# Kernel tuning notes

Measured on AMD Instinct MI355X. Metric: run time of the kernel, lower is better.

## Reference

```python
import jax, jax.numpy as jnp
import numpy as np

C_FEAT = 512
HID = 256
OUT = 3
IN_DIM = C_FEAT + 2 + 2  # feat + rel_coord + rel_cell = 516


def _nearest_idx(g, size):
    # grid_sample nearest, align_corners=False: unnormalize then round (half-to-even)
    x = ((g + 1.0) * size - 1.0) / 2.0
    return jnp.clip(jnp.round(x).astype(jnp.int32), 0, size - 1)


def setup_inputs() -> dict:
    key = jax.random.key(0)
    ks = jax.random.split(key, 12)
    B, Q, H, W = 2, 65536, 48, 48
    feat = jax.random.normal(ks[0], (B, C_FEAT, H, W), dtype=jnp.float32)
    coord = jax.random.uniform(ks[1], (B, Q, 2), dtype=jnp.float32, minval=-1.0, maxval=1.0)
    cell = jnp.full((B, Q, 2), 2.0 / 256.0, dtype=jnp.float32)  # query at 256x256 output res
    def lin_init(k, fan_in, fan_out):
        s = 1.0 / np.sqrt(fan_in)
        return jax.random.uniform(k, (fan_in, fan_out), jnp.float32, -s, s)
    W0 = lin_init(ks[2], IN_DIM, HID); b0 = jnp.zeros((HID,), jnp.float32)
    W1 = lin_init(ks[3], HID, HID);    b1 = jnp.zeros((HID,), jnp.float32)
    W2 = lin_init(ks[4], HID, HID);    b2 = jnp.zeros((HID,), jnp.float32)
    W3 = lin_init(ks[5], HID, HID);    b3 = jnp.zeros((HID,), jnp.float32)
    W4 = lin_init(ks[6], HID, OUT);    b4 = jnp.zeros((OUT,), jnp.float32)
    return {"feat": feat, "coord": coord, "cell": cell,
            "W0": W0, "b0": b0, "W1": W1, "b1": b1, "W2": W2, "b2": b2,
            "W3": W3, "b3": b3, "W4": W4, "b4": b4}


def _liif(feat, coord, cell, W0, b0, W1, b1, W2, b2, W3, b3, W4, b4):
    B, C, H, W = feat.shape
    Q = coord.shape[1]
    rx = 1.0 / H  # 2 / H / 2
    ry = 1.0 / W
    eps = 1e-6
    # local ensemble shifts (vx, vy) in order [(-1,-1),(-1,1),(1,-1),(1,1)]
    shifts = jnp.array([[-1., -1.], [-1., 1.], [1., -1.], [1., 1.]], dtype=feat.dtype)
    off = shifts * jnp.array([rx, ry], dtype=feat.dtype) + eps  # [4,2]
    coord_s = jnp.clip(coord[None] + off[:, None, None, :], -1 + 1e-6, 1 - 1e-6)  # [4,B,Q,2]
    # coord[...,0] indexes H (rows), coord[...,1] indexes W (cols) [code flips before grid_sample]
    idx_r = _nearest_idx(coord_s[..., 0], H)  # [4,B,Q]
    idx_c = _nearest_idx(coord_s[..., 1], W)
    lin = idx_r * W + idx_c                   # [4,B,Q]
    flat = feat.reshape(B, C, H * W).transpose(0, 2, 1)  # [B,HW,C]
    q_feat = jnp.take_along_axis(flat[None], lin[..., None], axis=2)  # [4,B,Q,C]
    # feat_coord grid_sample == center coord of the gathered cell
    qc_r = (idx_r.astype(feat.dtype) + 0.5) * (2.0 / H) - 1.0
    qc_c = (idx_c.astype(feat.dtype) + 0.5) * (2.0 / W) - 1.0
    rel = jnp.stack([(coord[None, ..., 0] - qc_r) * H,
                     (coord[None, ..., 1] - qc_c) * W], axis=-1)  # [4,B,Q,2]
    rel_cell = cell * jnp.array([H, W], dtype=feat.dtype)          # [B,Q,2]
    rel_cell4 = jnp.broadcast_to(rel_cell[None], (4, B, Q, 2))
    inp = jnp.concatenate([q_feat, rel, rel_cell4], axis=-1)       # [4,B,Q,516]
    # shared per-point MLP
    h = jax.nn.relu(inp @ W0 + b0)
    h = jax.nn.relu(h @ W1 + b1)
    h = jax.nn.relu(h @ W2 + b2)
    h = jax.nn.relu(h @ W3 + b3)
    pred = h @ W4 + b4                                             # [4,B,Q,3]
    area = jnp.abs(rel[..., 0] * rel[..., 1]) + 1e-9               # [4,B,Q]
    tot = area.sum(axis=0)
    # swap areas 0<->3 and 1<->2 (diagonal weighting) == reverse
    w = area[::-1] / tot[None]
    return (pred * w[..., None]).sum(axis=0)                       # [B,Q,3]


def reference(feat, coord, cell, W0, b0, W1, b1, W2, b2, W3, b3, W4, b4):
    return _liif(feat, coord, cell, W0, b0, W1, b1, W2, b2, W3, b3, W4, b4)
```

## Files before the change

kernel.cpp:

```cpp
#include <hip/hip_runtime.h>
#include <hip/hip_bf16.h>
#include <math.h>

#define HH    48
#define CFEAT 512
#define HID   256
#define NPOS  (HH*HH)
#define TQ    48
#define NEV   192
#define NB    1366

typedef __attribute__((ext_vector_type(8))) short bf16x8;
typedef __attribute__((ext_vector_type(4))) float f32x4;

static __device__ __forceinline__ unsigned short f2bf(float x) {
  unsigned int u = __float_as_uint(x);
  u += 0x7fffu + ((u >> 16) & 1u);
  return (unsigned short)(u >> 16);
}

static __device__ __forceinline__ unsigned int pk2bf(float a, float b) {
  __hip_bfloat162 h2 = __float22bfloat162_rn(make_float2(a, b));
  unsigned int u; __builtin_memcpy(&u, &h2, 4); return u;
}

static __device__ __forceinline__ void rel_calc(float c0, float c1, int s,
                                                float& r0, float& r1,
                                                int& ir, int& ic) {
  float vx = (s & 2) ? 1.0f : -1.0f;
  float vy = (s & 1) ? 1.0f : -1.0f;
  const float RXY = (float)(1.0/48.0);
  const float CLO = (float)(-1.0 + 1e-6);
  const float CHI = (float)( 1.0 - 1e-6);
  float gx = __fadd_rn(c0, __fadd_rn(__fmul_rn(vx, RXY), 1e-6f));
  float gy = __fadd_rn(c1, __fadd_rn(__fmul_rn(vy, RXY), 1e-6f));
  gx = fminf(fmaxf(gx, CLO), CHI);
  gy = fminf(fmaxf(gy, CLO), CHI);
  float xr = __fmul_rn(__fsub_rn(__fmul_rn(__fadd_rn(gx, 1.0f), 48.0f), 1.0f), 0.5f);
  float xc = __fmul_rn(__fsub_rn(__fmul_rn(__fadd_rn(gy, 1.0f), 48.0f), 1.0f), 0.5f);
  ir = (int)rintf(xr); ir = ir < 0 ? 0 : (ir > HH-1 ? HH-1 : ir);
  ic = (int)rintf(xc); ic = ic < 0 ? 0 : (ic > HH-1 ? HH-1 : ic);
  const float T2 = (float)(2.0/48.0);
  float qcr = __fsub_rn(__fmul_rn(__fadd_rn((float)ir, 0.5f), T2), 1.0f);
  float qcc = __fsub_rn(__fmul_rn(__fadd_rn((float)ic, 0.5f), T2), 1.0f);
  r0 = __fmul_rn(__fsub_rn(c0, qcr), 48.0f);
  r1 = __fmul_rn(__fsub_rn(c1, qcc), 48.0f);
}

__global__ __launch_bounds__(256) void liif_precompute(
    const float* __restrict__ feat, const float* __restrict__ W0,
    const float* __restrict__ b0, float* __restrict__ P)
{
  int blk = blockIdx.x;
  int b   = blk / (NPOS/4);
  int p0  = (blk - b*(NPOS/4)) * 4;
  int n   = threadIdx.x;
  const float* f = feat + (size_t)b * CFEAT * NPOS + p0;
  float bias = b0[n];
  float a0 = bias, a1 = bias, a2 = bias, a3 = bias;
  #pragma unroll 4
  for (int c = 0; c < CFEAT; ++c) {
    float w = W0[c*HID + n];
    const float* fr = f + (size_t)c * NPOS;
    a0 += fr[0]*w; a1 += fr[1]*w; a2 += fr[2]*w; a3 += fr[3]*w;
  }
  float* Pp = P + ((size_t)b*NPOS + p0)*HID + n;
  Pp[0*HID] = a0; Pp[1*HID] = a1; Pp[2*HID] = a2; Pp[3*HID] = a3;
}

__global__ __launch_bounds__(256) void liif_convert(
    const float* __restrict__ W1, const float* __restrict__ W2,
    const float* __restrict__ W3, const float* __restrict__ W4,
    unsigned char* __restrict__ img, unsigned char* __restrict__ w4i)
{
  int blk = blockIdx.x, t = threadIdx.x;
  if (blk < 24) {
    int l = blk >> 3, kc = blk & 7;
    const float* W = (l == 0) ? W1 : (l == 1) ? W2 : W3;
    unsigned short* dst = (unsigned short*)(img + (size_t)blk * 16384);
    #pragma unroll 1
    for (int s = 0; s < 4; ++s) {
      int p    = t + s*256;
      int wc   = p >> 8;
      int nt   = (p >> 6) & 3;
      int lane = p & 63;
      int lr   = lane & 15, lk = lane >> 4;
      int n    = wc*64 + nt*16 + lr;
      int k0   = kc*32 + lk*8;
      #pragma unroll
      for (int j = 0; j < 8; ++j)
        dst[p*8 + j] = f2bf(W[(k0 + j)*256 + n]);
    }
  } else {
    unsigned short* dst = (unsigned short*)w4i;
    #pragma unroll
    for (int u = 0; u < 2; ++u) {
      int p    = t + u*256;
      int kc   = p >> 6;
      int lane = p & 63;
      int n    = lane & 15;
      int k0   = kc*32 + (lane >> 4)*8;
      #pragma unroll
      for (int j = 0; j < 8; ++j)
        dst[p*8 + j] = (n < 3) ? f2bf(W4[(k0 + j)*3 + n]) : (unsigned short)0;
    }
  }
}


#define WBASE  98304

#define MF(A, B, C) __builtin_amdgcn_mfma_f32_16x16x32_bf16((A), (B), (C), 0, 0, 0)

#define AS1(p) ((const __attribute__((address_space(1))) void*)(unsigned long long)(const void*)(p))
#define AS3(p) ((__attribute__((address_space(3))) void*)(unsigned int)(unsigned long long)(void*)(p))

#define STAGEG(GOFF, BUF) do {                                                \
    __builtin_amdgcn_global_load_lds(                                         \
        AS1(img + (GOFF) + sgoff),                                            \
        AS3(lds + WBASE + (BUF)*32768 + swoff), 16, 0, 0);                    \
    __builtin_amdgcn_global_load_lds(                                         \
        AS1(img + (GOFF) + 12288 + sgoff),                                    \
        AS3(lds + WBASE + (BUF)*32768 + 12288 + swoff), 16, 0, 0);            \
    if (w < 8)                                                                \
      __builtin_amdgcn_global_load_lds(                                       \
          AS1(img + (GOFF) + 24576 + sgoff),                                  \
          AS3(lds + WBASE + (BUF)*32768 + 24576 + swoff), 16, 0, 0);          \
  } while (0)

#define KSTEPC(KC) do {                                                       \
    const unsigned char* wb_ = lds + WBASE + (((KC) >> 1) & 1)*32768          \
                             + (((KC) & 1)*16384) + lwoff;                    \
    bf16x8 w0_ = *(const bf16x8*)(wb_ + 0);                                   \
    bf16x8 w1_ = *(const bf16x8*)(wb_ + 1024);                                \
    bf16x8 w2_ = *(const bf16x8*)(wb_ + 2048);                                \
    bf16x8 w3_ = *(const bf16x8*)(wb_ + 3072);                                \
    const int ko_ = (((KC) << 6) ^ xb6);                                      \
    bf16x8 a0_ = *(const bf16x8*)(lds + rb0 + ko_);                           \
    bf16x8 a1_ = *(const bf16x8*)(lds + rb1 + ko_);                           \
    bf16x8 a2_ = *(const bf16x8*)(lds + rb2 + ko_);                           \
    bf16x8 a3_ = *(const bf16x8*)(lds + rb3 + ko_);                           \
    acc[0]  = MF(w0_, a0_, acc[0]);  acc[1]  = MF(w1_, a0_, acc[1]);          \
    acc[2]  = MF(w2_, a0_, acc[2]);  acc[3]  = MF(w3_, a0_, acc[3]);          \
    acc[4]  = MF(w0_, a1_, acc[4]);  acc[5]  = MF(w1_, a1_, acc[5]);          \
    acc[6]  = MF(w2_, a1_, acc[6]);  acc[7]  = MF(w3_, a1_, acc[7]);          \
    acc[8]  = MF(w0_, a2_, acc[8]);  acc[9]  = MF(w1_, a2_, acc[9]);          \
    acc[10] = MF(w2_, a2_, acc[10]); acc[11] = MF(w3_, a2_, acc[11]);         \
    acc[12] = MF(w0_, a3_, acc[12]); acc[13] = MF(w1_, a3_, acc[13]);         \
    acc[14] = MF(w2_, a3_, acc[14]); acc[15] = MF(w3_, a3_, acc[15]);         \
  } while (0)

#define LGROUP(G, HASN, NGOFF) do {                                           \
    if (HASN) STAGEG((NGOFF), (((G)+1)&1));                                   \
    KSTEPC(2*(G)); KSTEPC(2*(G)+1);                                           \
    __syncthreads();                                                          \
  } while (0)

#define LAYERC3(LOFF, NLOFF) do {                                             \
    _Pragma("unroll")                                                         \
    for (int i_ = 0; i_ < 16; ++i_) acc[i_] = (f32x4){0.f, 0.f, 0.f, 0.f};    \
    LGROUP(0, 1, (LOFF) + 32768);                                             \
    LGROUP(1, 1, (LOFF) + 65536);                                             \
    LGROUP(2, 1, (LOFF) + 98304);                                             \
    LGROUP(3, 1, (NLOFF));                                                    \
  } while (0)

#define LAYER_WB3(BIAS) do {                                                  \
    _Pragma("unroll")                                                         \
    for (int nt_ = 0; nt_ < 4; ++nt_) {                                       \
      f32x4 bv_ = *(const f32x4*)&(BIAS)[nW + nt_*16 + lk*4];                 \
      const int cb_ = (cwb + nt_*32) ^ xwb;                                   \
      _Pragma("unroll")                                                       \
      for (int mt_ = 0; mt_ < 4; ++mt_) {                                     \
        f32x4 a_ = acc[mt_*4 + nt_];                                          \
        unsigned int lo_ = pk2bf(fmaxf(a_[0] + bv_[0], 0.f),                  \
                                 fmaxf(a_[1] + bv_[1], 0.f));                 \
        unsigned int hi_ = pk2bf(fmaxf(a_[2] + bv_[2], 0.f),                  \
                                 fmaxf(a_[3] + bv_[3], 0.f));                 \
        *(uint2*)(lds + ((m0 + mt_*16 + lr) << 9) + cb_) = make_uint2(lo_, hi_); \
      }                                                                       \
    }                                                                         \
  } while (0)

__global__ __launch_bounds__(768, 3)
__attribute__((amdgpu_waves_per_eu(3, 3)))
void liif_main(
    const float* __restrict__ coord, const float* __restrict__ cell,
    const float* __restrict__ P,  const float* __restrict__ W0,
    const unsigned char* __restrict__ img,
    const unsigned char* __restrict__ w4i,
    const float* __restrict__ b1, const float* __restrict__ b2,
    const float* __restrict__ b3, const float* __restrict__ b4,
    float* __restrict__ out)
{
  __shared__ __align__(16) unsigned char lds[163840];
  int*   lin_s = (int*)  (lds + WBASE);
  f32x4* rel4  = (f32x4*)(lds + WBASE + 1024);
  float* predp = (float*)lds;

  const int t   = threadIdx.x;
  const int blk = blockIdx.x;
  const int b   = (blk >= NB) ? 1 : 0;
  const int q0  = (blk - b*NB) * TQ;

  const int lane = t & 63;
  const int w    = t >> 6;
  const int m0   = (w >> 2) * 64;
  const int wc   = w & 3;
  const int nW   = wc * 64;
  const int lr   = lane & 15;
  const int lk   = lane >> 4;

  const size_t sgoff = (size_t)t * 16;
  const int    swoff = w * 1024;

  const int lwoff = wc*4096 + lane*16;
  const int xl  = (lr & 3) << 4;
  const int xb6 = ((lr >> 2) & 1) << 6;
  const int rb0 = ((m0 +  0 + lr) << 9) + ((lk << 4) ^ xl);
  const int rb1 = ((m0 + 16 + lr) << 9) + ((lk << 4) ^ xl);
  const int rb2 = ((m0 + 32 + lr) << 9) + ((lk << 4) ^ xl);
  const int rb3 = ((m0 + 48 + lr) << 9) + ((lk << 4) ^ xl);
  const int cwb = wc*128 + lk*8;
  const int xwb = (lr & 7) << 4;

  if (t < NEV) {
    const int e = t;
    int q = q0 + (e >> 2);
    if (q > 65535) q = 65535;
    const int s = e & 3;
    const size_t cbase = (((size_t)b << 16) + q) * 2;
    float c0 = coord[cbase + 0];
    float c1 = coord[cbase + 1];
    float r0, r1; int ir, ic;
    rel_calc(c0, c1, s, r0, r1, ir, ic);
    lin_s[e] = ir*HH + ic;
    rel4[e] = (f32x4){r0, r1,
                      __fmul_rn(cell[cbase + 0], 48.0f),
                      __fmul_rn(cell[cbase + 1], 48.0f)};
  }
  __syncthreads();

  {
    const int cg = lane;
    const float* w0t = W0 + (size_t)512*HID + cg*4;
    f32x4 wr0 = *(const f32x4*)(w0t);
    f32x4 wr1 = *(const f32x4*)(w0t + 256);
    f32x4 wr2 = *(const f32x4*)(w0t + 512);
    f32x4 wr3 = *(const f32x4*)(w0t + 768);
    const float* Pb = P + (size_t)b * NPOS * HID + cg*4;
    const int wb = cg * 8;
    #pragma unroll 2
    for (int i = 0; i < 16; ++i) {
      const int e = w*16 + i;
      const int lin = lin_s[e];
      f32x4 rel = rel4[e];
      f32x4 pv = *(const f32x4*)(Pb + (size_t)lin*HID);
      float v0 = pv[0] + rel[0]*wr0[0] + rel[1]*wr1[0] + rel[2]*wr2[0] + rel[3]*wr3[0];
      float v1 = pv[1] + rel[0]*wr0[1] + rel[1]*wr1[1] + rel[2]*wr2[1] + rel[3]*wr3[1];
      float v2 = pv[2] + rel[0]*wr0[2] + rel[1]*wr1[2] + rel[2]*wr2[2] + rel[3]*wr3[2];
      float v3 = pv[3] + rel[0]*wr0[3] + rel[1]*wr1[3] + rel[2]*wr2[3] + rel[3]*wr3[3];
      unsigned int lo = pk2bf(fmaxf(v0, 0.f), fmaxf(v1, 0.f));
      unsigned int hi = pk2bf(fmaxf(v2, 0.f), fmaxf(v3, 0.f));
      *(uint2*)(lds + (e << 9) + (wb ^ ((e & 7) << 4))) = make_uint2(lo, hi);
    }
  }
  __syncthreads();

  STAGEG(0, 0);
  __syncthreads();

  f32x4 acc[16];
  LAYERC3(0, 131072);
  LAYER_WB3(b1);
  __syncthreads();

  LAYERC3(131072, 262144);
  LAYER_WB3(b2);
  __syncthreads();

  {
    #pragma unroll
    for (int i_ = 0; i_ < 16; ++i_) acc[i_] = (f32x4){0.f, 0.f, 0.f, 0.f};
    LGROUP(0, 1, 262144 + 32768);
    LGROUP(1, 1, 262144 + 65536);
    LGROUP(2, 1, 262144 + 98304);
    if (w < 8)
      __builtin_amdgcn_global_load_lds(AS1(w4i + sgoff),
                                       AS3(lds + WBASE + swoff), 16, 0, 0);
    KSTEPC(6); KSTEPC(7);
    __syncthreads();
  }
  LAYER_WB3(b3);
  __syncthreads();

  {
    f32x4 acc4 = (f32x4){0.f, 0.f, 0.f, 0.f};
    const int fr_ = ((w << 4) + lr) << 9;
    #pragma unroll
    for (int kc = 0; kc < 8; ++kc) {
      bf16x8 wf = *(const bf16x8*)(lds + WBASE + kc*1024 + lane*16);
      bf16x8 af = *(const bf16x8*)(lds + fr_ + ((kc << 6) ^ xb6) + ((lk << 4) ^ xl));
      acc4 = MF(wf, af, acc4);
    }
    __syncthreads();
    if (lk == 0) {
      float* pp = predp + ((w << 4) + lr)*3;
      pp[0] = acc4[0] + b4[0];
      pp[1] = acc4[1] + b4[1];
      pp[2] = acc4[2] + b4[2];
    }
  }
  __syncthreads();

  if (t < TQ*3) {
    const int q = t / 3, o = t - (t/3)*3;
    const int qq = q0 + q;
    if (qq < 65536) {
      const int eb = q*4;
      const size_t cbase = (((size_t)b << 16) + qq) * 2;
      float c0 = coord[cbase + 0];
      float c1 = coord[cbase + 1];
      float ar[4];
      #pragma unroll
      for (int s = 0; s < 4; ++s) {
        float r0, r1; int ir, ic;
        rel_calc(c0, c1, s, r0, r1, ir, ic);
        ar[s] = __fadd_rn(fabsf(__fmul_rn(r0, r1)), 1e-9f);
      }
      float p0 = predp[(eb+0)*3 + o];
      float p1 = predp[(eb+1)*3 + o];
      float p2 = predp[(eb+2)*3 + o];
      float p3 = predp[(eb+3)*3 + o];
      float tot = ((ar[0] + ar[1]) + ar[2]) + ar[3];
      float rv = (p0*ar[3] + p1*ar[2] + p2*ar[1] + p3*ar[0]) / tot;
      out[(((size_t)b << 16) + qq)*3 + o] = rv;
    }
  }
}

extern "C" void kernel_launch(void* const* d_in, const int* in_sizes, int n_in,
                              void* d_out, int out_size, void* d_ws, size_t ws_size,
                              hipStream_t stream)
{
  const float* feat  = (const float*)d_in[0];
  const float* coord = (const float*)d_in[1];
  const float* cell  = (const float*)d_in[2];
  const float* W0    = (const float*)d_in[3];
  const float* b0    = (const float*)d_in[4];
  const float* W1    = (const float*)d_in[5];
  const float* b1    = (const float*)d_in[6];
  const float* W2    = (const float*)d_in[7];
  const float* b2    = (const float*)d_in[8];
  const float* W3    = (const float*)d_in[9];
  const float* b3    = (const float*)d_in[10];
  const float* W4    = (const float*)d_in[11];
  const float* b4    = (const float*)d_in[12];
  float* outp = (float*)d_out;

  float*         P    = (float*)d_ws;
  unsigned char* imgp = (unsigned char*)d_ws + 4718592;
  unsigned char* w4ip = (unsigned char*)d_ws + 4718592 + 393216;

  hipLaunchKernelGGL(liif_precompute, dim3(2*(NPOS/4)), dim3(256), 0, stream,
                     feat, W0, b0, P);
  hipLaunchKernelGGL(liif_convert, dim3(25), dim3(256), 0, stream,
                     W1, W2, W3, W4, imgp, w4ip);
  hipLaunchKernelGGL(liif_main, dim3(2*NB), dim3(768), 0, stream,
                     coord, cell, P, W0, imgp, w4ip, b1, b2, b3, b4, outp);
}
```

Before: 280.6 us.

## Retile main MLP kernel to 64 queries, 8 waves, 64x128 per-wave tiles

Changes the query tile from 48 to 64 points (256 evaluations), so blocks divide the query count evenly and bounds checks can be removed. Each of 8 waves now computes a 64x128 output tile with 32 accumulators, where it used to be 12 waves doing 64x64 tiles. Weight staging becomes per-k-step double buffering of 16KB chunks, issued before the first-layer gather so it overlaps that phase. The intent is more MFMA work per LDS weight load and fewer waves contending. The cost is higher register pressure, occupancy dropping to 2 waves/EU, and a sync after every k-step.

```diff
diff --git a/kernel.cpp b/kernel.cpp
--- a/kernel.cpp
+++ b/kernel.cpp
@@ -6,9 +6,8 @@
 #define CFEAT 512
 #define HID   256
 #define NPOS  (HH*HH)
-#define TQ    48
-#define NEV   192
-#define NB    1366
+#define TQ    64
+#define NEV   256
 
 typedef __attribute__((ext_vector_type(8))) short bf16x8;
 typedef __attribute__((ext_vector_type(4))) float f32x4;
@@ -108,33 +107,33 @@
 }
 
 
-#define WBASE  98304
+#define LDSW   131072
 
 #define MF(A, B, C) __builtin_amdgcn_mfma_f32_16x16x32_bf16((A), (B), (C), 0, 0, 0)
 
 #define AS1(p) ((const __attribute__((address_space(1))) void*)(unsigned long long)(const void*)(p))
 #define AS3(p) ((__attribute__((address_space(3))) void*)(unsigned int)(unsigned long long)(void*)(p))
 
-#define STAGEG(GOFF, BUF) do {                                                \
+#define STAGE2(LOFF, NKC, BUF) do {                                           \
     __builtin_amdgcn_global_load_lds(                                         \
-        AS1(img + (GOFF) + sgoff),                                            \
-        AS3(lds + WBASE + (BUF)*32768 + swoff), 16, 0, 0);                    \
+        AS1(img + (LOFF) + (NKC)*16384 + sgoff),                              \
+        AS3(lds + LDSW + (BUF)*16384 + swoff), 16, 0, 0);                     \
     __builtin_amdgcn_global_load_lds(                                         \
-        AS1(img + (GOFF) + 12288 + sgoff),                                    \
-        AS3(lds + WBASE + (BUF)*32768 + 12288 + swoff), 16, 0, 0);            \
-    if (w < 8)                                                                \
-      __builtin_amdgcn_global_load_lds(                                       \
-          AS1(img + (GOFF) + 24576 + sgoff),                                  \
-          AS3(lds + WBASE + (BUF)*32768 + 24576 + swoff), 16, 0, 0);          \
+        AS1(img + (LOFF) + (NKC)*16384 + sgoff + 8192),                       \
+        AS3(lds + LDSW + (BUF)*16384 + swoff + 8192), 16, 0, 0);              \
   } while (0)
 
-#define KSTEPC(KC) do {                                                       \
-    const unsigned char* wb_ = lds + WBASE + (((KC) >> 1) & 1)*32768          \
-                             + (((KC) & 1)*16384) + lwoff;                    \
+#define KSTEP32(KC, HASN, NLOFF, NKC) do {                                    \
+    if (HASN) STAGE2((NLOFF), (NKC), (((KC)+1)&1));                           \
+    const unsigned char* wb_ = lds + LDSW + (((KC)&1)*16384) + lwoff;         \
     bf16x8 w0_ = *(const bf16x8*)(wb_ + 0);                                   \
     bf16x8 w1_ = *(const bf16x8*)(wb_ + 1024);                                \
     bf16x8 w2_ = *(const bf16x8*)(wb_ + 2048);                                \
     bf16x8 w3_ = *(const bf16x8*)(wb_ + 3072);                                \
+    bf16x8 w4_ = *(const bf16x8*)(wb_ + 4096);                                \
+    bf16x8 w5_ = *(const bf16x8*)(wb_ + 5120);                                \
+    bf16x8 w6_ = *(const bf16x8*)(wb_ + 6144);                                \
+    bf16x8 w7_ = *(const bf16x8*)(wb_ + 7168);                                \
     const int ko_ = (((KC) << 6) ^ xb6);                                      \
     bf16x8 a0_ = *(const bf16x8*)(lds + rb0 + ko_);                           \
     bf16x8 a1_ = *(const bf16x8*)(lds + rb1 + ko_);                           \
@@ -142,37 +141,40 @@
     bf16x8 a3_ = *(const bf16x8*)(lds + rb3 + ko_);                           \
     acc[0]  = MF(w0_, a0_, acc[0]);  acc[1]  = MF(w1_, a0_, acc[1]);          \
     acc[2]  = MF(w2_, a0_, acc[2]);  acc[3]  = MF(w3_, a0_, acc[3]);          \
-    acc[4]  = MF(w0_, a1_, acc[4]);  acc[5]  = MF(w1_, a1_, acc[5]);          \
-    acc[6]  = MF(w2_, a1_, acc[6]);  acc[7]  = MF(w3_, a1_, acc[7]);          \
-    acc[8]  = MF(w0_, a2_, acc[8]);  acc[9]  = MF(w1_, a2_, acc[9]);          \
-    acc[10] = MF(w2_, a2_, acc[10]); acc[11] = MF(w3_, a2_, acc[11]);         \
-    acc[12] = MF(w0_, a3_, acc[12]); acc[13] = MF(w1_, a3_, acc[13]);         \
-    acc[14] = MF(w2_, a3_, acc[14]); acc[15] = MF(w3_, a3_, acc[15]);         \
-  } while (0)
-
-#define LGROUP(G, HASN, NGOFF) do {                                           \
-    if (HASN) STAGEG((NGOFF), (((G)+1)&1));                                   \
-    KSTEPC(2*(G)); KSTEPC(2*(G)+1);                                           \
+    acc[4]  = MF(w4_, a0_, acc[4]);  acc[5]  = MF(w5_, a0_, acc[5]);          \
+    acc[6]  = MF(w6_, a0_, acc[6]);  acc[7]  = MF(w7_, a0_, acc[7]);          \
+    acc[8]  = MF(w0_, a1_, acc[8]);  acc[9]  = MF(w1_, a1_, acc[9]);          \
+    acc[10] = MF(w2_, a1_, acc[10]); acc[11] = MF(w3_, a1_, acc[11]);         \
+    acc[12] = MF(w4_, a1_, acc[12]); acc[13] = MF(w5_, a1_, acc[13]);         \
+    acc[14] = MF(w6_, a1_, acc[14]); acc[15] = MF(w7_, a1_, acc[15]);         \
+    acc[16] = MF(w0_, a2_, acc[16]); acc[17] = MF(w1_, a2_, acc[17]);         \
+    acc[18] = MF(w2_, a2_, acc[18]); acc[19] = MF(w3_, a2_, acc[19]);         \
+    acc[20] = MF(w4_, a2_, acc[20]); acc[21] = MF(w5_, a2_, acc[21]);         \
+    acc[22] = MF(w6_, a2_, acc[22]); acc[23] = MF(w7_, a2_, acc[23]);         \
+    acc[24] = MF(w0_, a3_, acc[24]); acc[25] = MF(w1_, a3_, acc[25]);         \
+    acc[26] = MF(w2_, a3_, acc[26]); acc[27] = MF(w3_, a3_, acc[27]);         \
+    acc[28] = MF(w4_, a3_, acc[28]); acc[29] = MF(w5_, a3_, acc[29]);         \
+    acc[30] = MF(w6_, a3_, acc[30]); acc[31] = MF(w7_, a3_, acc[31]);         \
     __syncthreads();                                                          \
   } while (0)
 
-#define LAYERC3(LOFF, NLOFF) do {                                             \
+#define LAYER32(LOFF, NLOFF) do {                                             \
     _Pragma("unroll")                                                         \
-    for (int i_ = 0; i_ < 16; ++i_) acc[i_] = (f32x4){0.f, 0.f, 0.f, 0.f};    \
-    LGROUP(0, 1, (LOFF) + 32768);                                             \
-    LGROUP(1, 1, (LOFF) + 65536);                                             \
-    LGROUP(2, 1, (LOFF) + 98304);                                             \
-    LGROUP(3, 1, (NLOFF));                                                    \
+    for (int i_ = 0; i_ < 32; ++i_) acc[i_] = (f32x4){0.f, 0.f, 0.f, 0.f};    \
+    KSTEP32(0, 1, (LOFF), 1); KSTEP32(1, 1, (LOFF), 2);                       \
+    KSTEP32(2, 1, (LOFF), 3); KSTEP32(3, 1, (LOFF), 4);                       \
+    KSTEP32(4, 1, (LOFF), 5); KSTEP32(5, 1, (LOFF), 6);                       \
+    KSTEP32(6, 1, (LOFF), 7); KSTEP32(7, 1, (NLOFF), 0);                      \
   } while (0)
 
-#define LAYER_WB3(BIAS) do {                                                  \
+#define LAYER_WB(BIAS) do {                                                   \
     _Pragma("unroll")                                                         \
-    for (int nt_ = 0; nt_ < 4; ++nt_) {                                       \
+    for (int nt_ = 0; nt_ < 8; ++nt_) {                                       \
       f32x4 bv_ = *(const f32x4*)&(BIAS)[nW + nt_*16 + lk*4];                 \
       const int cb_ = (cwb + nt_*32) ^ xwb;                                   \
       _Pragma("unroll")                                                       \
       for (int mt_ = 0; mt_ < 4; ++mt_) {                                     \
-        f32x4 a_ = acc[mt_*4 + nt_];                                          \
+        f32x4 a_ = acc[mt_*8 + nt_];                                          \
         unsigned int lo_ = pk2bf(fmaxf(a_[0] + bv_[0], 0.f),                  \
                                  fmaxf(a_[1] + bv_[1], 0.f));                 \
         unsigned int hi_ = pk2bf(fmaxf(a_[2] + bv_[2], 0.f),                  \
@@ -182,8 +184,8 @@
     }                                                                         \
   } while (0)
 
-__global__ __launch_bounds__(768, 3)
-__attribute__((amdgpu_waves_per_eu(3, 3)))
+__global__ __launch_bounds__(512, 2)
+__attribute__((amdgpu_waves_per_eu(2, 2)))
 void liif_main(
     const float* __restrict__ coord, const float* __restrict__ cell,
     const float* __restrict__ P,  const float* __restrict__ W0,
@@ -194,40 +196,38 @@
     float* __restrict__ out)
 {
   __shared__ __align__(16) unsigned char lds[163840];
-  int*   lin_s = (int*)  (lds + WBASE);
-  f32x4* rel4  = (f32x4*)(lds + WBASE + 1024);
+  int*   lin_s = (int*)  (lds + 147456);
+  f32x4* rel4  = (f32x4*)(lds + 147456 + 1024);
   float* predp = (float*)lds;
 
   const int t   = threadIdx.x;
   const int blk = blockIdx.x;
-  const int b   = (blk >= NB) ? 1 : 0;
-  const int q0  = (blk - b*NB) * TQ;
+  const int b   = blk >> 10;
+  const int q0  = (blk & 1023) * TQ;
 
   const int lane = t & 63;
   const int w    = t >> 6;
-  const int m0   = (w >> 2) * 64;
-  const int wc   = w & 3;
-  const int nW   = wc * 64;
+  const int m0   = (w >> 1) * 64;
+  const int nW   = (w & 1) * 128;
   const int lr   = lane & 15;
   const int lk   = lane >> 4;
 
   const size_t sgoff = (size_t)t * 16;
   const int    swoff = w * 1024;
 
-  const int lwoff = wc*4096 + lane*16;
+  const int lwoff = (w & 1)*8192 + lane*16;
   const int xl  = (lr & 3) << 4;
   const int xb6 = ((lr >> 2) & 1) << 6;
   const int rb0 = ((m0 +  0 + lr) << 9) + ((lk << 4) ^ xl);
   const int rb1 = ((m0 + 16 + lr) << 9) + ((lk << 4) ^ xl);
   const int rb2 = ((m0 + 32 + lr) << 9) + ((lk << 4) ^ xl);
   const int rb3 = ((m0 + 48 + lr) << 9) + ((lk << 4) ^ xl);
-  const int cwb = wc*128 + lk*8;
+  const int cwb = (w & 1)*256 + lk*8;
   const int xwb = (lr & 7) << 4;
 
   if (t < NEV) {
     const int e = t;
-    int q = q0 + (e >> 2);
-    if (q > 65535) q = 65535;
+    const int q = q0 + (e >> 2);
     const int s = e & 3;
     const size_t cbase = (((size_t)b << 16) + q) * 2;
     float c0 = coord[cbase + 0];
@@ -241,6 +241,8 @@
   }
   __syncthreads();
 
+  STAGE2(0, 0, 0);
+
   {
     const int cg = lane;
     const float* w0t = W0 + (size_t)512*HID + cg*4;
@@ -251,8 +253,8 @@
     const float* Pb = P + (size_t)b * NPOS * HID + cg*4;
     const int wb = cg * 8;
     #pragma unroll 2
-    for (int i = 0; i < 16; ++i) {
-      const int e = w*16 + i;
+    for (int i = 0; i < 32; ++i) {
+      const int e = w*32 + i;
       const int lin = lin_s[e];
       f32x4 rel = rel4[e];
       f32x4 pv = *(const f32x4*)(Pb + (size_t)lin*HID);
@@ -267,75 +269,73 @@
   }
   __syncthreads();
 
-  STAGEG(0, 0);
-  __syncthreads();
-
-  f32x4 acc[16];
-  LAYERC3(0, 131072);
-  LAYER_WB3(b1);
-  __syncthreads();
-
-  LAYERC3(131072, 262144);
-  LAYER_WB3(b2);
+  f32x4 acc[32];
+  LAYER32(0, 131072);
+  LAYER_WB(b1);
+  __syncthreads();
+
+  LAYER32(131072, 262144);
+  LAYER_WB(b2);
   __syncthreads();
 
   {
     #pragma unroll
-    for (int i_ = 0; i_ < 16; ++i_) acc[i_] = (f32x4){0.f, 0.f, 0.f, 0.f};
-    LGROUP(0, 1, 262144 + 32768);
-    LGROUP(1, 1, 262144 + 65536);
-    LGROUP(2, 1, 262144 + 98304);
-    if (w < 8)
-      __builtin_amdgcn_global_load_lds(AS1(w4i + sgoff),
-                                       AS3(lds + WBASE + swoff), 16, 0, 0);
-    KSTEPC(6); KSTEPC(7);
-    __syncthreads();
-  }
-  LAYER_WB3(b3);
+    for (int i_ = 0; i_ < 32; ++i_) acc[i_] = (f32x4){0.f, 0.f, 0.f, 0.f};
+    KSTEP32(0, 1, 262144, 1); KSTEP32(1, 1, 262144, 2);
+    KSTEP32(2, 1, 262144, 3); KSTEP32(3, 1, 262144, 4);
+    KSTEP32(4, 1, 262144, 5); KSTEP32(5, 1, 262144, 6);
+    KSTEP32(6, 1, 262144, 7);
+    __builtin_amdgcn_global_load_lds(AS1(w4i + sgoff),
+                                     AS3(lds + LDSW + swoff), 16, 0, 0);
+    KSTEP32(7, 0, 0, 0);
+  }
+  LAYER_WB(b3);
   __syncthreads();
 
   {
-    f32x4 acc4 = (f32x4){0.f, 0.f, 0.f, 0.f};
-    const int fr_ = ((w << 4) + lr) << 9;
+    f32x4 acc4a = (f32x4){0.f, 0.f, 0.f, 0.f};
+    f32x4 acc4b = (f32x4){0.f, 0.f, 0.f, 0.f};
+    const int fr0 = ((w*32)      + lr) << 9;
+    const int fr1 = ((w*32 + 16) + lr) << 9;
     #pragma unroll
     for (int kc = 0; kc < 8; ++kc) {
-      bf16x8 wf = *(const bf16x8*)(lds + WBASE + kc*1024 + lane*16);
-      bf16x8 af = *(const bf16x8*)(lds + fr_ + ((kc << 6) ^ xb6) + ((lk << 4) ^ xl));
-      acc4 = MF(wf, af, acc4);
+      bf16x8 wf = *(const bf16x8*)(lds + LDSW + kc*1024 + lane*16);
+      const int ko = ((kc << 6) ^ xb6) + ((lk << 4) ^ xl);
+      bf16x8 afa = *(const bf16x8*)(lds + fr0 + ko);
+      bf16x8 afb = *(const bf16x8*)(lds + fr1 + ko);
+      acc4a = MF(wf, afa, acc4a);
+      acc4b = MF(wf, afb, acc4b);
     }
     __syncthreads();
     if (lk == 0) {
-      float* pp = predp + ((w << 4) + lr)*3;
-      pp[0] = acc4[0] + b4[0];
-      pp[1] = acc4[1] + b4[1];
-      pp[2] = acc4[2] + b4[2];
+      float* pa = predp + (w*32 + lr)*3;
+      float* pb = predp + (w*32 + 16 + lr)*3;
+      pa[0] = acc4a[0] + b4[0]; pa[1] = acc4a[1] + b4[1]; pa[2] = acc4a[2] + b4[2];
+      pb[0] = acc4b[0] + b4[0]; pb[1] = acc4b[1] + b4[1]; pb[2] = acc4b[2] + b4[2];
     }
   }
   __syncthreads();
 
   if (t < TQ*3) {
     const int q = t / 3, o = t - (t/3)*3;
-    const int qq = q0 + q;
-    if (qq < 65536) {
-      const int eb = q*4;
-      const size_t cbase = (((size_t)b << 16) + qq) * 2;
-      float c0 = coord[cbase + 0];
-      float c1 = coord[cbase + 1];
-      float ar[4];
-      #pragma unroll
-      for (int s = 0; s < 4; ++s) {
-        float r0, r1; int ir, ic;
-        rel_calc(c0, c1, s, r0, r1, ir, ic);
-        ar[s] = __fadd_rn(fabsf(__fmul_rn(r0, r1)), 1e-9f);
-      }
-      float p0 = predp[(eb+0)*3 + o];
-      float p1 = predp[(eb+1)*3 + o];
-      float p2 = predp[(eb+2)*3 + o];
-      float p3 = predp[(eb+3)*3 + o];
-      float tot = ((ar[0] + ar[1]) + ar[2]) + ar[3];
-      float rv = (p0*ar[3] + p1*ar[2] + p2*ar[1] + p3*ar[0]) / tot;
-      out[(((size_t)b << 16) + qq)*3 + o] = rv;
-    }
+    const int eb = q*4;
+    const size_t cbase = (((size_t)b << 16) + (q0 + q)) * 2;
+    float c0 = coord[cbase + 0];
+    float c1 = coord[cbase + 1];
+    float ar[4];
+    #pragma unroll
+    for (int s = 0; s < 4; ++s) {
+      float r0, r1; int ir, ic;
+      rel_calc(c0, c1, s, r0, r1, ir, ic);
+      ar[s] = __fadd_rn(fabsf(__fmul_rn(r0, r1)), 1e-9f);
+    }
+    float p0 = predp[(eb+0)*3 + o];
+    float p1 = predp[(eb+1)*3 + o];
+    float p2 = predp[(eb+2)*3 + o];
+    float p3 = predp[(eb+3)*3 + o];
+    float tot = ((ar[0] + ar[1]) + ar[2]) + ar[3];
+    float rv = (p0*ar[3] + p1*ar[2] + p2*ar[1] + p3*ar[0]) / tot;
+    out[(((size_t)b << 16) + (q0 + q))*3 + o] = rv;
   }
 }
 
@@ -366,6 +366,6 @@
                      feat, W0, b0, P);
   hipLaunchKernelGGL(liif_convert, dim3(25), dim3(256), 0, stream,
                      W1, W2, W3, W4, imgp, w4ip);
-  hipLaunchKernelGGL(liif_main, dim3(2*NB), dim3(768), 0, stream,
+  hipLaunchKernelGGL(liif_main, dim3(2048), dim3(512), 0, stream,
                      coord, cell, P, W0, imgp, w4ip, b1, b2, b3, b4, outp);
 }
```

Result: slower. 298.4 us (+6.3%).

## Software-pipeline MLP layers with per-k-chunk weight staging and register double-buffering

Applied to the files above, without the earlier changes.

Restructures the hidden-layer GEMM loop so weights are staged one 16KB k-chunk at a time into a two-slot LDS ring, while fragments for the next chunk are loaded into registers (even/odd sets) as the MFMAs for the current chunk issue. MFMA blocks are wrapped in s_setprio raises, and the first layer's weight staging is issued before the layer-0 gather so it overlaps that work. LDS use drops from 160KB to 128KB, but the change doubles the number of barriers per layer and adds register pressure from the extra fragment buffers.

```diff
diff --git a/kernel.cpp b/kernel.cpp
--- a/kernel.cpp
+++ b/kernel.cpp
@@ -108,64 +108,47 @@
 }
 
 
-#define WBASE  98304
+#define LDSW   98304
 
 #define MF(A, B, C) __builtin_amdgcn_mfma_f32_16x16x32_bf16((A), (B), (C), 0, 0, 0)
 
 #define AS1(p) ((const __attribute__((address_space(1))) void*)(unsigned long long)(const void*)(p))
 #define AS3(p) ((__attribute__((address_space(3))) void*)(unsigned int)(unsigned long long)(void*)(p))
 
-#define STAGEG(GOFF, BUF) do {                                                \
+#define STAGEC(LOFF, KC, BUF) do {                                            \
     __builtin_amdgcn_global_load_lds(                                         \
-        AS1(img + (GOFF) + sgoff),                                            \
-        AS3(lds + WBASE + (BUF)*32768 + swoff), 16, 0, 0);                    \
-    __builtin_amdgcn_global_load_lds(                                         \
-        AS1(img + (GOFF) + 12288 + sgoff),                                    \
-        AS3(lds + WBASE + (BUF)*32768 + 12288 + swoff), 16, 0, 0);            \
-    if (w < 8)                                                                \
+        AS1(img + (LOFF) + (KC)*16384 + sgoff),                               \
+        AS3(lds + LDSW + (BUF)*16384 + swoff), 16, 0, 0);                     \
+    if (w < 4)                                                                \
       __builtin_amdgcn_global_load_lds(                                       \
-          AS1(img + (GOFF) + 24576 + sgoff),                                  \
-          AS3(lds + WBASE + (BUF)*32768 + 24576 + swoff), 16, 0, 0);          \
-  } while (0)
-
-#define KSTEPC(KC) do {                                                       \
-    const unsigned char* wb_ = lds + WBASE + (((KC) >> 1) & 1)*32768          \
-                             + (((KC) & 1)*16384) + lwoff;                    \
-    bf16x8 w0_ = *(const bf16x8*)(wb_ + 0);                                   \
-    bf16x8 w1_ = *(const bf16x8*)(wb_ + 1024);                                \
-    bf16x8 w2_ = *(const bf16x8*)(wb_ + 2048);                                \
-    bf16x8 w3_ = *(const bf16x8*)(wb_ + 3072);                                \
-    const int ko_ = (((KC) << 6) ^ xb6);                                      \
-    bf16x8 a0_ = *(const bf16x8*)(lds + rb0 + ko_);                           \
-    bf16x8 a1_ = *(const bf16x8*)(lds + rb1 + ko_);                           \
-    bf16x8 a2_ = *(const bf16x8*)(lds + rb2 + ko_);                           \
-    bf16x8 a3_ = *(const bf16x8*)(lds + rb3 + ko_);                           \
-    acc[0]  = MF(w0_, a0_, acc[0]);  acc[1]  = MF(w1_, a0_, acc[1]);          \
-    acc[2]  = MF(w2_, a0_, acc[2]);  acc[3]  = MF(w3_, a0_, acc[3]);          \
-    acc[4]  = MF(w0_, a1_, acc[4]);  acc[5]  = MF(w1_, a1_, acc[5]);          \
-    acc[6]  = MF(w2_, a1_, acc[6]);  acc[7]  = MF(w3_, a1_, acc[7]);          \
-    acc[8]  = MF(w0_, a2_, acc[8]);  acc[9]  = MF(w1_, a2_, acc[9]);          \
-    acc[10] = MF(w2_, a2_, acc[10]); acc[11] = MF(w3_, a2_, acc[11]);         \
-    acc[12] = MF(w0_, a3_, acc[12]); acc[13] = MF(w1_, a3_, acc[13]);         \
-    acc[14] = MF(w2_, a3_, acc[14]); acc[15] = MF(w3_, a3_, acc[15]);         \
-  } while (0)
-
-#define LGROUP(G, HASN, NGOFF) do {                                           \
-    if (HASN) STAGEG((NGOFF), (((G)+1)&1));                                   \
-    KSTEPC(2*(G)); KSTEPC(2*(G)+1);                                           \
-    __syncthreads();                                                          \
-  } while (0)
-
-#define LAYERC3(LOFF, NLOFF) do {                                             \
+          AS1(img + (LOFF) + (KC)*16384 + 12288 + sgoff),                     \
+          AS3(lds + LDSW + (BUF)*16384 + 12288 + swoff), 16, 0, 0);           \
+  } while (0)
+
+#define RD(AARR, WARR, KC) do {                                               \
+    const unsigned char* wbp_ = lds + LDSW + (((KC)&1)*16384) + lwoff;        \
+    WARR[0] = *(const bf16x8*)(wbp_ + 0);                                     \
+    WARR[1] = *(const bf16x8*)(wbp_ + 1024);                                  \
+    WARR[2] = *(const bf16x8*)(wbp_ + 2048);                                  \
+    WARR[3] = *(const bf16x8*)(wbp_ + 3072);                                  \
+    const int ko_ = (((KC) << 6) ^ xb6) + ((lk << 4) ^ xl);                   \
+    AARR[0] = *(const bf16x8*)(lds + ((m0 +  0 + lr) << 9) + ko_);            \
+    AARR[1] = *(const bf16x8*)(lds + ((m0 + 16 + lr) << 9) + ko_);            \
+    AARR[2] = *(const bf16x8*)(lds + ((m0 + 32 + lr) << 9) + ko_);            \
+    AARR[3] = *(const bf16x8*)(lds + ((m0 + 48 + lr) << 9) + ko_);            \
+  } while (0)
+
+#define MM(WARR, AARR) do {                                                   \
+    __builtin_amdgcn_s_setprio(1);                                            \
     _Pragma("unroll")                                                         \
-    for (int i_ = 0; i_ < 16; ++i_) acc[i_] = (f32x4){0.f, 0.f, 0.f, 0.f};    \
-    LGROUP(0, 1, (LOFF) + 32768);                                             \
-    LGROUP(1, 1, (LOFF) + 65536);                                             \
-    LGROUP(2, 1, (LOFF) + 98304);                                             \
-    LGROUP(3, 1, (NLOFF));                                                    \
-  } while (0)
-
-#define LAYER_WB3(BIAS) do {                                                  \
+    for (int m_ = 0; m_ < 4; ++m_)                                            \
+      _Pragma("unroll")                                                       \
+      for (int n_ = 0; n_ < 4; ++n_)                                          \
+        acc[m_*4 + n_] = MF(WARR[n_], AARR[m_], acc[m_*4 + n_]);              \
+    __builtin_amdgcn_s_setprio(0);                                            \
+  } while (0)
+
+#define LAYER_WB(BIAS) do {                                                   \
     _Pragma("unroll")                                                         \
     for (int nt_ = 0; nt_ < 4; ++nt_) {                                       \
       f32x4 bv_ = *(const f32x4*)&(BIAS)[nW + nt_*16 + lk*4];                 \
@@ -182,6 +165,30 @@
     }                                                                         \
   } while (0)
 
+#define LAYERP(LOFF, NLOFF, ISL3) do {                                        \
+    RD(aE, wE, 0);                                                            \
+    _Pragma("unroll")                                                         \
+    for (int i_ = 0; i_ < 16; ++i_) acc[i_] = (f32x4){0.f, 0.f, 0.f, 0.f};    \
+    __syncthreads(); STAGEC((LOFF), 2, 0); RD(aO, wO, 1); MM(wE, aE);   \
+    __syncthreads(); STAGEC((LOFF), 3, 1); RD(aE, wE, 2); MM(wO, aO);   \
+    __syncthreads(); STAGEC((LOFF), 4, 0); RD(aO, wO, 3); MM(wE, aE);   \
+    __syncthreads(); STAGEC((LOFF), 5, 1); RD(aE, wE, 4); MM(wO, aO);   \
+    __syncthreads(); STAGEC((LOFF), 6, 0); RD(aO, wO, 5); MM(wE, aE);   \
+    __syncthreads(); STAGEC((LOFF), 7, 1); RD(aE, wE, 6); MM(wO, aO);   \
+    __syncthreads();                                                    \
+    if (ISL3) {                                                               \
+      if (w < 8)                                                              \
+        __builtin_amdgcn_global_load_lds(AS1(w4i + sgoff),                    \
+                                         AS3(lds + LDSW + swoff), 16, 0, 0);  \
+    } else {                                                                  \
+      STAGEC((NLOFF), 0, 0);                                                  \
+    }                                                                         \
+    RD(aO, wO, 7); MM(wE, aE);                                                \
+    __syncthreads();                                                    \
+    if (!(ISL3)) STAGEC((NLOFF), 1, 1);                                       \
+    MM(wO, aO);                                                               \
+  } while (0)
+
 __global__ __launch_bounds__(768, 3)
 __attribute__((amdgpu_waves_per_eu(3, 3)))
 void liif_main(
@@ -193,9 +200,9 @@
     const float* __restrict__ b3, const float* __restrict__ b4,
     float* __restrict__ out)
 {
-  __shared__ __align__(16) unsigned char lds[163840];
-  int*   lin_s = (int*)  (lds + WBASE);
-  f32x4* rel4  = (f32x4*)(lds + WBASE + 1024);
+  __shared__ __align__(16) unsigned char lds[131072];
+  int*   lin_s = (int*)  (lds + 114688);
+  f32x4* rel4  = (f32x4*)(lds + 114688 + 1024);
   float* predp = (float*)lds;
 
   const int t   = threadIdx.x;
@@ -217,10 +224,6 @@
   const int lwoff = wc*4096 + lane*16;
   const int xl  = (lr & 3) << 4;
   const int xb6 = ((lr >> 2) & 1) << 6;
-  const int rb0 = ((m0 +  0 + lr) << 9) + ((lk << 4) ^ xl);
-  const int rb1 = ((m0 + 16 + lr) << 9) + ((lk << 4) ^ xl);
-  const int rb2 = ((m0 + 32 + lr) << 9) + ((lk << 4) ^ xl);
-  const int rb3 = ((m0 + 48 + lr) << 9) + ((lk << 4) ^ xl);
   const int cwb = wc*128 + lk*8;
   const int xwb = (lr & 7) << 4;
 
@@ -240,6 +243,8 @@
                       __fmul_rn(cell[cbase + 1], 48.0f)};
   }
   __syncthreads();
+
+  STAGEC(0, 0, 0);
 
   {
     const int cg = lane;
@@ -267,31 +272,21 @@
   }
   __syncthreads();
 
-  STAGEG(0, 0);
-  __syncthreads();
+  STAGEC(0, 1, 1);
 
   f32x4 acc[16];
-  LAYERC3(0, 131072);
-  LAYER_WB3(b1);
-  __syncthreads();
-
-  LAYERC3(131072, 262144);
-  LAYER_WB3(b2);
-  __syncthreads();
-
-  {
-    #pragma unroll
-    for (int i_ = 0; i_ < 16; ++i_) acc[i_] = (f32x4){0.f, 0.f, 0.f, 0.f};
-    LGROUP(0, 1, 262144 + 32768);
-    LGROUP(1, 1, 262144 + 65536);
-    LGROUP(2, 1, 262144 + 98304);
-    if (w < 8)
-      __builtin_amdgcn_global_load_lds(AS1(w4i + sgoff),
-                                       AS3(lds + WBASE + swoff), 16, 0, 0);
-    KSTEPC(6); KSTEPC(7);
-    __syncthreads();
-  }
-  LAYER_WB3(b3);
+  bf16x8 wE[4], aE[4], wO[4], aO[4];
+
+  LAYERP(0, 131072, 0);
+  LAYER_WB(b1);
+  __syncthreads();
+
+  LAYERP(131072, 262144, 0);
+  LAYER_WB(b2);
+  __syncthreads();
+
+  LAYERP(262144, 0, 1);
+  LAYER_WB(b3);
   __syncthreads();
 
   {
@@ -299,7 +294,7 @@
     const int fr_ = ((w << 4) + lr) << 9;
     #pragma unroll
     for (int kc = 0; kc < 8; ++kc) {
-      bf16x8 wf = *(const bf16x8*)(lds + WBASE + kc*1024 + lane*16);
+      bf16x8 wf = *(const bf16x8*)(lds + LDSW + kc*1024 + lane*16);
       bf16x8 af = *(const bf16x8*)(lds + fr_ + ((kc << 6) ^ xb6) + ((lk << 4) ^ xl));
       acc4 = MF(wf, af, acc4);
     }
```

New measurement: 299.6 us. +6.8%, slower.
